# Kernel tuning notes

Measured on AMD Instinct MI355X. Metric: run time of the kernel, lower is better.

Reference implementation:

```python
import jax, jax.numpy as jnp
import numpy as np

N_EMBD = 1024
N_HEAD = 16
D_HEAD = N_EMBD // N_HEAD
B, T = 4, 2048


def _layernorm(x, g, b, eps=1e-5):
    mu = jnp.mean(x, axis=-1, keepdims=True)
    var = jnp.var(x, axis=-1, keepdims=True)
    return (x - mu) * jax.lax.rsqrt(var + eps) * g + b


def setup_inputs() -> dict:
    key = jax.random.key(0)
    ks = jax.random.split(key, 16)
    C = N_EMBD
    s = 0.02
    return {
        "x": jax.random.normal(ks[0], (B, T, C), jnp.float32),
        "ln1_g": jnp.ones((C,), jnp.float32),
        "ln1_b": jnp.zeros((C,), jnp.float32),
        "Wq": jax.random.normal(ks[1], (C, C), jnp.float32) * s,
        "bq": jnp.zeros((C,), jnp.float32),
        "Wk": jax.random.normal(ks[2], (C, C), jnp.float32) * s,
        "bk": jnp.zeros((C,), jnp.float32),
        "Wv": jax.random.normal(ks[3], (C, C), jnp.float32) * s,
        "bv": jnp.zeros((C,), jnp.float32),
        "Wo": jax.random.normal(ks[4], (C, C), jnp.float32) * s,
        "bo": jnp.zeros((C,), jnp.float32),
        "ln2_g": jnp.ones((C,), jnp.float32),
        "ln2_b": jnp.zeros((C,), jnp.float32),
        "W1": jax.random.normal(ks[5], (C, 4 * C), jnp.float32) * s,
        "b1": jnp.zeros((4 * C,), jnp.float32),
        "W2": jax.random.normal(ks[6], (4 * C, C), jnp.float32) * s,
        "b2": jnp.zeros((C,), jnp.float32),
    }


def reference(x, ln1_g, ln1_b, Wq, bq, Wk, bk, Wv, bv, Wo, bo,
              ln2_g, ln2_b, W1, b1, W2, b2):
    Bx, Tx, C = x.shape
    H, D = N_HEAD, D_HEAD

    # --- attention (pre-LN) ---
    h = _layernorm(x, ln1_g, ln1_b)
    q = (h @ Wq + bq).reshape(Bx, Tx, H, D)
    k = (h @ Wk + bk).reshape(Bx, Tx, H, D)
    v = (h @ Wv + bv).reshape(Bx, Tx, H, D)
    att = jnp.einsum("bqhd,bkhd->bhqk", q, k) * (1.0 / jnp.sqrt(jnp.float32(D)))
    causal = jnp.tril(jnp.ones((Tx, Tx), bool))
    att = jnp.where(causal, att, -jnp.inf)
    att = jax.nn.softmax(att, axis=-1)
    y = jnp.einsum("bhqk,bkhd->bqhd", att, v).reshape(Bx, Tx, C)
    x = x + (y @ Wo + bo)

    # --- MLP (pre-LN), exact GELU as in torch F.gelu default ---
    h2 = _layernorm(x, ln2_g, ln2_b)
    m = jax.nn.gelu(h2 @ W1 + b1, approximate=False)
    x = x + (m @ W2 + b2)
    return x
```

## Files before the change

kernel.cpp:

```cpp
#include <hip/hip_runtime.h>
#include <hip/hip_bf16.h>
#include <math.h>

#define C_EMBD 1024
#define T_SEQ  2048
#define BATCH  4
#define NHEAD  16
#define DHEAD  64

typedef __attribute__((ext_vector_type(8))) short bf16x8;
typedef __attribute__((ext_vector_type(4))) float floatx4;

#if __has_builtin(__builtin_amdgcn_exp2f)
#define EXP2F __builtin_amdgcn_exp2f
#else
#define EXP2F exp2f
#endif

static __device__ __forceinline__ floatx4 mfma16(bf16x8 a, bf16x8 b, floatx4 c) {
    return __builtin_amdgcn_mfma_f32_16x16x32_bf16(a, b, c, 0, 0, 0);
}

static __device__ __forceinline__ void gl2lds16(const void* g, void* l) {
    __builtin_amdgcn_global_load_lds(
        (const __attribute__((address_space(1))) void*)g,
        (__attribute__((address_space(3))) void*)l, 16, 0, 0);
}

__global__ __launch_bounds__(256) void transpose_cvt(
        const float* __restrict__ W, __hip_bfloat16* __restrict__ Wt, int K, int N) {
    __shared__ float tile[32][33];
    const int tid = threadIdx.x;
    const int n0 = blockIdx.x * 32, k0 = blockIdx.y * 32;
    const int r = tid >> 3, c4 = (tid & 7) * 4;
    float4 v = *(const float4*)&W[(size_t)(k0 + r) * N + n0 + c4];
    tile[r][c4 + 0] = v.x; tile[r][c4 + 1] = v.y;
    tile[r][c4 + 2] = v.z; tile[r][c4 + 3] = v.w;
    __syncthreads();
    __align__(8) __hip_bfloat16 ob[4];
    ob[0] = __float2bfloat16(tile[c4 + 0][r]);
    ob[1] = __float2bfloat16(tile[c4 + 1][r]);
    ob[2] = __float2bfloat16(tile[c4 + 2][r]);
    ob[3] = __float2bfloat16(tile[c4 + 3][r]);
    *(short4*)&Wt[(size_t)(n0 + r) * K + k0 + c4] = *(short4*)ob;
}

__global__ __launch_bounds__(256) void ln_bf16(
        const float* __restrict__ x, const float* __restrict__ g,
        const float* __restrict__ b, __hip_bfloat16* __restrict__ out) {
    const int row = blockIdx.x, tid = threadIdx.x;
    const float4 v = ((const float4*)(x + (size_t)row * C_EMBD))[tid];
    float s  = v.x + v.y + v.z + v.w;
    float sq = v.x * v.x + v.y * v.y + v.z * v.z + v.w * v.w;
    #pragma unroll
    for (int off = 1; off < 64; off <<= 1) {
        s  += __shfl_xor(s, off);
        sq += __shfl_xor(sq, off);
    }
    __shared__ float ps[4], pq[4];
    if ((tid & 63) == 0) { ps[tid >> 6] = s; pq[tid >> 6] = sq; }
    __syncthreads();
    s  = ps[0] + ps[1] + ps[2] + ps[3];
    sq = pq[0] + pq[1] + pq[2] + pq[3];
    const float mu   = s * (1.0f / C_EMBD);
    const float var  = sq * (1.0f / C_EMBD) - mu * mu;
    const float rstd = rsqrtf(var + 1e-5f);
    const float4 gv = ((const float4*)g)[tid];
    const float4 bv = ((const float4*)b)[tid];
    __align__(8) __hip_bfloat16 ob[4];
    ob[0] = __float2bfloat16((v.x - mu) * rstd * gv.x + bv.x);
    ob[1] = __float2bfloat16((v.y - mu) * rstd * gv.y + bv.y);
    ob[2] = __float2bfloat16((v.z - mu) * rstd * gv.z + bv.z);
    ob[3] = __float2bfloat16((v.w - mu) * rstd * gv.w + bv.w);
    *(short4*)&out[(size_t)row * C_EMBD + tid * 4] = *(short4*)ob;
}

template <int EP>
__global__ __launch_bounds__(256, 2) void gemm_bt(
        const __hip_bfloat16* __restrict__ A, const __hip_bfloat16* __restrict__ Bt,
        int M, int N, int K,
        const float* __restrict__ ba, const float* __restrict__ bb, const float* __restrict__ bc,
        __hip_bfloat16* __restrict__ o0, __hip_bfloat16* __restrict__ o1,
        __hip_bfloat16* __restrict__ o2, float* __restrict__ of,
        const float* __restrict__ resid) {
    __shared__ __align__(16) __hip_bfloat16 As[2][128 * 32];
    __shared__ __align__(16) __hip_bfloat16 Bs[2][128 * 32];
    const int tid  = threadIdx.x;

    const int gx  = gridDim.x;
    const int nwg = gx * gridDim.y;
    const int lin = blockIdx.x + gx * blockIdx.y;
    const int cpx = nwg >> 3;
    const int wg  = (lin & 7) * cpx + (lin >> 3);
    const int by  = (wg & 7) + 8 * (wg / (gx << 3));
    const int bx  = (wg >> 3) % gx;
    const int n0  = bx * 128;
    const int m0  = by * 128;

    const int wave = tid >> 6, lane = tid & 63;
    const int l15  = lane & 15, quad = lane >> 4;
    const int wm   = (wave & 1) * 64, wn = (wave >> 1) * 64;
    const int c0   = wave * 2;
    const int sr   = lane >> 2;
    const int sc   = (lane & 3) * 8;

    const floatx4 z4 = {0.f, 0.f, 0.f, 0.f};
    floatx4 acc[4][4];
    #pragma unroll
    for (int i = 0; i < 4; i++)
        #pragma unroll
        for (int j = 0; j < 4; j++) acc[i][j] = z4;

    auto stage = [&](const int buf, const int k0) {
        gl2lds16(&A [(m0 + c0 * 16 + sr) * K + k0 + sc],       &As[buf][c0 * 512]);
        gl2lds16(&A [(m0 + (c0 + 1) * 16 + sr) * K + k0 + sc], &As[buf][(c0 + 1) * 512]);
        gl2lds16(&Bt[(n0 + c0 * 16 + sr) * K + k0 + sc],       &Bs[buf][c0 * 512]);
        gl2lds16(&Bt[(n0 + (c0 + 1) * 16 + sr) * K + k0 + sc], &Bs[buf][(c0 + 1) * 512]);
    };

    stage(0, 0);
    const int nk = K >> 5;
    for (int t = 0; t < nk; ++t) {
        const int cur = t & 1;
        if (t + 1 < nk) {
            stage(cur ^ 1, (t + 1) * 32);
            asm volatile("s_waitcnt vmcnt(4)" ::: "memory");
        } else {
            asm volatile("s_waitcnt vmcnt(0)" ::: "memory");
        }
        __builtin_amdgcn_s_barrier();
        asm volatile("" ::: "memory");
        bf16x8 af[4], bfr[4];
        #pragma unroll
        for (int i = 0; i < 4; i++)
            af[i] = *(const bf16x8*)&As[cur][(wm + i * 16 + l15) * 32 + quad * 8];
        #pragma unroll
        for (int j = 0; j < 4; j++)
            bfr[j] = *(const bf16x8*)&Bs[cur][(wn + j * 16 + l15) * 32 + quad * 8];
        #pragma unroll
        for (int i = 0; i < 4; i++)
            #pragma unroll
            for (int j = 0; j < 4; j++)
                acc[i][j] = mfma16(af[i], bfr[j], acc[i][j]);
        asm volatile("" ::: "memory");
        __builtin_amdgcn_s_barrier();
    }

    #pragma unroll
    for (int i = 0; i < 4; i++) {
        #pragma unroll
        for (int j = 0; j < 4; j++) {
            const int col = n0 + wn + j * 16 + l15;
            #pragma unroll
            for (int r = 0; r < 4; r++) {
                const int m = m0 + wm + i * 16 + quad * 4 + r;
                float val = acc[i][j][r];
                if (EP == 1) {
                    val += ba[col];
                    of[m * N + col] = resid[m * N + col] + val;
                } else {
                    val += ba[col];
                    of[m * N + col] += val;
                }
            }
        }
    }
}

template <int EP>
__global__ __launch_bounds__(512, 2) void gemm256_8ph(
        const __hip_bfloat16* __restrict__ A, const __hip_bfloat16* __restrict__ Bt,
        int M, int N, int K,
        const float* __restrict__ ba, const float* __restrict__ bb, const float* __restrict__ bc,
        __hip_bfloat16* __restrict__ o0, __hip_bfloat16* __restrict__ o1,
        __hip_bfloat16* __restrict__ o2) {
    __shared__ __align__(16) __hip_bfloat16 As[2][256 * 64];
    __shared__ __align__(16) __hip_bfloat16 Bs[2][256 * 64];
    const int tid = threadIdx.x;

    const int gx  = gridDim.x;
    const int nwg = gx * gridDim.y;
    const int lin = blockIdx.x + gx * blockIdx.y;
    const int cpx = nwg >> 3;
    const int wg  = (lin & 7) * cpx + (lin >> 3);
    const int by  = (wg & 7) + 8 * (wg / (gx << 3));
    const int bx  = (wg >> 3) % gx;
    const int n0  = bx * 256;
    const int m0  = by * 256;

    const int wave = tid >> 6, lane = tid & 63;
    const int l15 = lane & 15, quad = lane >> 4;
    const int wr  = wave >> 2, wc = wave & 3;
    const int swz = l15 & 7;
    const int sr8 = tid >> 3;
    const int sg  = (tid & 7) ^ (sr8 & 7);

    const floatx4 z4 = {0.f, 0.f, 0.f, 0.f};
    floatx4 acc[8][4];
    #pragma unroll
    for (int i = 0; i < 8; i++)
        #pragma unroll
        for (int j = 0; j < 4; j++) acc[i][j] = z4;

    auto stA = [&](const int buf, const int half, const int k0) {
        #pragma unroll
        for (int s = 0; s < 2; s++) {
            const int r0 = half * 128 + s * 64;
            gl2lds16(&A[(size_t)(m0 + r0 + sr8) * K + k0 + sg * 8],
                     &As[buf][r0 * 64 + wave * 512]);
        }
    };
    auto stB = [&](const int buf, const int half, const int k0) {
        #pragma unroll
        for (int s = 0; s < 2; s++) {
            const int r0 = half * 128 + s * 64;
            gl2lds16(&Bt[(size_t)(n0 + r0 + sr8) * K + k0 + sg * 8],
                     &Bs[buf][r0 * 64 + wave * 512]);
        }
    };
    auto ldA = [&](const int buf, const int mi, const int ks) -> bf16x8 {
        return *(const bf16x8*)&As[buf][(mi * 32 + wr * 16 + l15) * 64 +
                                        (((ks * 4 + quad) ^ swz) * 8)];
    };
    auto ldB = [&](const int buf, const int nj, const int ks) -> bf16x8 {
        return *(const bf16x8*)&Bs[buf][(wc * 64 + nj * 16 + l15) * 64 +
                                        (((ks * 4 + quad) ^ swz) * 8)];
    };

    const int NT = K >> 6;
    stA(0, 0, 0); stB(0, 0, 0); stA(0, 1, 0); stB(0, 1, 0);
    stA(1, 0, 64); stB(1, 0, 64);
    asm volatile("s_waitcnt vmcnt(4)" ::: "memory");
    __builtin_amdgcn_s_barrier();
    asm volatile("" ::: "memory");

    for (int t = 0; t < NT; ++t) {
        const int cur = t & 1;
        const int kn1 = (t + 1) * 64, kn2 = (t + 2) * 64;
        const bool s1 = (t + 1 < NT), s2 = (t + 2 < NT);
        bf16x8 bfrag[4][2];
        #pragma unroll
        for (int p = 0; p < 4; ++p) {
            bf16x8 afr[2][2];
            if (p == 0) {
                #pragma unroll
                for (int nj = 0; nj < 4; nj++)
                    #pragma unroll
                    for (int ks = 0; ks < 2; ks++)
                        bfrag[nj][ks] = ldB(cur, nj, ks);
            }
            #pragma unroll
            for (int i = 0; i < 2; i++)
                #pragma unroll
                for (int ks = 0; ks < 2; ks++)
                    afr[i][ks] = ldA(cur, 2 * p + i, ks);
            if (p == 0)      { if (s1) stA(cur ^ 1, 1, kn1); }
            else if (p == 1) { if (s1) stB(cur ^ 1, 1, kn1); }
            else if (p == 2) { if (s2) stA(cur, 0, kn2); }
            else             { if (s2) stB(cur, 0, kn2); }
            asm volatile("" ::: "memory");
            __builtin_amdgcn_s_barrier();
            asm volatile("s_waitcnt lgkmcnt(0)" ::: "memory");
            __builtin_amdgcn_s_setprio(1);
            #pragma unroll
            for (int i = 0; i < 2; i++)
                #pragma unroll
                for (int nj = 0; nj < 4; nj++)
                    #pragma unroll
                    for (int ks = 0; ks < 2; ks++)
                        acc[2 * p + i][nj] = mfma16(afr[i][ks], bfrag[nj][ks], acc[2 * p + i][nj]);
            __builtin_amdgcn_s_setprio(0);
            if (p == 3) {
                if (s2) { asm volatile("s_waitcnt vmcnt(4)" ::: "memory"); }
                else    { asm volatile("s_waitcnt vmcnt(0)" ::: "memory"); }
            }
            asm volatile("" ::: "memory");
            __builtin_amdgcn_s_barrier();
            asm volatile("" ::: "memory");
        }
    }

    #pragma unroll
    for (int mi = 0; mi < 8; mi++) {
        #pragma unroll
        for (int nj = 0; nj < 4; nj++) {
            const int col = n0 + wc * 64 + nj * 16 + l15;
            #pragma unroll
            for (int r = 0; r < 4; r++) {
                const int m = m0 + mi * 32 + wr * 16 + quad * 4 + r;
                float val = acc[mi][nj][r];
                if (EP == 0) {
                    const int which = col >> 10, cn = col & 1023;
                    const float* bp = (which == 0) ? ba : (which == 1) ? bb : bc;
                    val += bp[cn];
                    const int head = cn >> 6, d = cn & 63;
                    const int bidx = m >> 11, tt = m & 2047;
                    if (which == 0) {
                        val *= 0.18033688011112042f;
                        o0[((bidx * NHEAD + head) * T_SEQ + tt) * DHEAD + d] = __float2bfloat16(val);
                    } else if (which == 1) {
                        o1[((bidx * NHEAD + head) * T_SEQ + tt) * DHEAD + d] = __float2bfloat16(val);
                    } else {
                        o2[((bidx * NHEAD + head) * DHEAD + d) * T_SEQ + tt] = __float2bfloat16(val);
                    }
                } else {
                    val += ba[col];
                    const float gl = 0.5f * val * (1.0f + erff(val * 0.70710678118654752f));
                    o0[(size_t)m * N + col] = __float2bfloat16(gl);
                }
            }
        }
    }
}

__global__ __launch_bounds__(256, 2) void attn_fa(
        const __hip_bfloat16* __restrict__ q, const __hip_bfloat16* __restrict__ k,
        const __hip_bfloat16* __restrict__ vt, __hip_bfloat16* __restrict__ y) {
    __shared__ __align__(16) __hip_bfloat16 Ks[2][64 * 64];
    __shared__ __align__(16) __hip_bfloat16 Vs[2][64 * 64];
    __shared__ __align__(16) __hip_bfloat16 pl[4][32 * 72];
    const int tid = threadIdx.x;
    const int wave = tid >> 6, lane = tid & 63;
    const int l15 = lane & 15, quad = lane >> 4;
    const int sw  = l15 & 7;
    const int lr  = lane >> 3;
    const int gsw = (lane & 7) ^ lr;

    const int lin  = blockIdx.x;
    const int xcd  = lin & 7;
    const int slot = lin >> 3;
    const int bh   = xcd * 8 + (slot >> 3);
    const int jA   = slot & 7;

    const __hip_bfloat16* qp = q + (size_t)bh * T_SEQ * DHEAD;
    const __hip_bfloat16* kp = k + (size_t)bh * T_SEQ * DHEAD;
    const __hip_bfloat16* vp = vt + (size_t)bh * DHEAD * T_SEQ;
    __hip_bfloat16* myp = &pl[wave][0];
    const int b = bh >> 4, head = bh & 15;
    const floatx4 z4 = {0.f, 0.f, 0.f, 0.f};

    auto stage = [&](const int buf, const int kb) {
        #pragma unroll
        for (int j = 0; j < 2; j++) {
            const int rb = wave * 16 + j * 8;
            gl2lds16(&kp[(size_t)(kb + rb + lr) * DHEAD + gsw * 8], &Ks[buf][rb * 64]);
            gl2lds16(&vp[(size_t)(rb + lr) * T_SEQ + kb + gsw * 8], &Vs[buf][rb * 64]);
        }
    };

    auto segment = [&](const int tile) {
        const int q0 = tile * 128;
        const int qw = q0 + wave * 32;
        const int cc = tile * 2 + 1;

        bf16x8 bq[2][2];
        #pragma unroll
        for (int qi = 0; qi < 2; qi++)
            #pragma unroll
            for (int h = 0; h < 2; h++)
                bq[qi][h] = *(const bf16x8*)&qp[(qw + qi * 16 + l15) * DHEAD + h * 32 + quad * 8];

        floatx4 oac[2][4];
        #pragma unroll
        for (int qi = 0; qi < 2; qi++)
            #pragma unroll
            for (int nd = 0; nd < 4; nd++) oac[qi][nd] = z4;
        float li[2] = {0.f, 0.f};

        stage(0, 0);

        for (int t = 0; t <= cc; t++) {
            const int cur = t & 1;
            if (t < cc) {
                stage(cur ^ 1, (t + 1) * 64);
                asm volatile("s_waitcnt vmcnt(4)" ::: "memory");
            } else {
                asm volatile("s_waitcnt vmcnt(0)" ::: "memory");
            }
            __builtin_amdgcn_s_barrier();
            asm volatile("" ::: "memory");

            const int kb = t * 64;
            const bool act = (kb <= qw + 31);
            if (act) {
                const bool dg = (kb + 63 > qw);
                bf16x8 kf[4][2];
                #pragma unroll
                for (int nt = 0; nt < 4; nt++)
                    #pragma unroll
                    for (int h = 0; h < 2; h++)
                        kf[nt][h] = *(const bf16x8*)&Ks[cur][(nt * 16 + l15) * 64 + (((h * 4 + quad) ^ sw) * 8)];
                floatx4 sa[2][4];
                #pragma unroll
                for (int qi = 0; qi < 2; qi++)
                    #pragma unroll
                    for (int nt = 0; nt < 4; nt++) sa[qi][nt] = z4;
                #pragma unroll
                for (int nt = 0; nt < 4; nt++)
                    #pragma unroll
                    for (int h = 0; h < 2; h++) {
                        sa[0][nt] = mfma16(kf[nt][h], bq[0][h], sa[0][nt]);
                        sa[1][nt] = mfma16(kf[nt][h], bq[1][h], sa[1][nt]);
                    }
                if (dg) {
                    #pragma unroll
                    for (int qi = 0; qi < 2; qi++)
                        #pragma unroll
                        for (int nt = 0; nt < 4; nt++)
                            #pragma unroll
                            for (int r = 0; r < 4; r++)
                                if (kb + nt * 16 + quad * 4 + r > qw + qi * 16 + l15)
                                    sa[qi][nt][r] = -INFINITY;
                }
                #pragma unroll
                for (int qi = 0; qi < 2; qi++) {
                    float sm = 0.f;
                    #pragma unroll
                    for (int nt = 0; nt < 4; nt++) {
                        __align__(8) __hip_bfloat16 pk[4];
                        #pragma unroll
                        for (int r = 0; r < 4; r++) {
                            const float p = EXP2F(sa[qi][nt][r]);
                            sm += p;
                            pk[r] = __float2bfloat16(p);
                        }
                        *(short4*)&myp[(qi * 16 + l15) * 72 + nt * 16 + quad * 4] = *(short4*)pk;
                    }
                    li[qi] += sm;
                }
                bf16x8 vf[4][2];
                #pragma unroll
                for (int nd = 0; nd < 4; nd++)
                    #pragma unroll
                    for (int kh = 0; kh < 2; kh++)
                        vf[nd][kh] = *(const bf16x8*)&Vs[cur][(nd * 16 + l15) * 64 + (((kh * 4 + quad) ^ sw) * 8)];
                asm volatile("s_waitcnt lgkmcnt(0)" ::: "memory");
                bf16x8 pf[2][2];
                #pragma unroll
                for (int qi = 0; qi < 2; qi++)
                    #pragma unroll
                    for (int kh = 0; kh < 2; kh++)
                        pf[qi][kh] = *(const bf16x8*)&myp[(qi * 16 + l15) * 72 + kh * 32 + quad * 8];
                #pragma unroll
                for (int nd = 0; nd < 4; nd++)
                    #pragma unroll
                    for (int kh = 0; kh < 2; kh++) {
                        oac[0][nd] = mfma16(vf[nd][kh], pf[0][kh], oac[0][nd]);
                        oac[1][nd] = mfma16(vf[nd][kh], pf[1][kh], oac[1][nd]);
                    }
            }
            asm volatile("" ::: "memory");
            __builtin_amdgcn_s_barrier();
        }

        float inv[2];
        #pragma unroll
        for (int qi = 0; qi < 2; qi++) {
            float l = li[qi];
            l += __shfl_xor(l, 16);
            l += __shfl_xor(l, 32);
            inv[qi] = 1.0f / l;
        }
        #pragma unroll
        for (int qi = 0; qi < 2; qi++)
            #pragma unroll
            for (int nd = 0; nd < 4; nd++) {
                __align__(8) __hip_bfloat16 ok[4];
                #pragma unroll
                for (int r = 0; r < 4; r++) ok[r] = __float2bfloat16(oac[qi][nd][r] * inv[qi]);
                *(short4*)&myp[(qi * 16 + l15) * 72 + nd * 16 + quad * 4] = *(short4*)ok;
            }
        asm volatile("s_waitcnt lgkmcnt(0)" ::: "memory");
        #pragma unroll
        for (int half = 0; half < 2; half++) {
            const int row = half * 16 + (lane >> 2);
            const int cb  = (lane & 3) * 16;
            const bf16x8 v0 = *(const bf16x8*)&myp[row * 72 + cb];
            const bf16x8 v1 = *(const bf16x8*)&myp[row * 72 + cb + 8];
            __hip_bfloat16* yr = &y[(size_t)(b * T_SEQ + qw + row) * C_EMBD + head * DHEAD + cb];
            *(bf16x8*)yr       = v0;
            *(bf16x8*)(yr + 8) = v1;
        }
        asm volatile("s_waitcnt vmcnt(0)" ::: "memory");
    };

    segment(jA);
    segment(15 - jA);
}

extern "C" void kernel_launch(void* const* d_in, const int* in_sizes, int n_in,
                              void* d_out, int out_size, void* d_ws, size_t ws_size,
                              hipStream_t stream) {
    const float* x     = (const float*)d_in[0];
    const float* ln1_g = (const float*)d_in[1];
    const float* ln1_b = (const float*)d_in[2];
    const float* Wq    = (const float*)d_in[3];
    const float* bq    = (const float*)d_in[4];
    const float* Wk    = (const float*)d_in[5];
    const float* bk    = (const float*)d_in[6];
    const float* Wv    = (const float*)d_in[7];
    const float* bv    = (const float*)d_in[8];
    const float* Wo    = (const float*)d_in[9];
    const float* bo    = (const float*)d_in[10];
    const float* ln2_g = (const float*)d_in[11];
    const float* ln2_b = (const float*)d_in[12];
    const float* W1    = (const float*)d_in[13];
    const float* b1    = (const float*)d_in[14];
    const float* W2    = (const float*)d_in[15];
    const float* b2    = (const float*)d_in[16];
    float* out = (float*)d_out;

    char* ws = (char*)d_ws;
    __hip_bfloat16* wqkvt = (__hip_bfloat16*)(ws);
    __hip_bfloat16* wot   = (__hip_bfloat16*)(ws + 6291456);
    __hip_bfloat16* w1t   = (__hip_bfloat16*)(ws + 8388608);
    __hip_bfloat16* w2t   = (__hip_bfloat16*)(ws + 16777216);
    __hip_bfloat16* hbuf  = (__hip_bfloat16*)(ws + 25165824);
    __hip_bfloat16* qbuf  = (__hip_bfloat16*)(ws + 41943040);
    __hip_bfloat16* kbuf  = (__hip_bfloat16*)(ws + 58720256);
    __hip_bfloat16* vbuf  = (__hip_bfloat16*)(ws + 75497472);
    __hip_bfloat16* ybuf  = (__hip_bfloat16*)(ws + 92274688);
    __hip_bfloat16* mbuf  = (__hip_bfloat16*)(ws + 41943040);

    transpose_cvt<<<dim3(32, 32), 256, 0, stream>>>(Wq, wqkvt, 1024, 1024);
    transpose_cvt<<<dim3(32, 32), 256, 0, stream>>>(Wk, wqkvt + 1024 * 1024, 1024, 1024);
    transpose_cvt<<<dim3(32, 32), 256, 0, stream>>>(Wv, wqkvt + 2048 * 1024, 1024, 1024);
    transpose_cvt<<<dim3(32, 32), 256, 0, stream>>>(Wo, wot, 1024, 1024);
    transpose_cvt<<<dim3(128, 32), 256, 0, stream>>>(W1, w1t, 1024, 4096);
    transpose_cvt<<<dim3(32, 128), 256, 0, stream>>>(W2, w2t, 4096, 1024);

    ln_bf16<<<8192, 256, 0, stream>>>(x, ln1_g, ln1_b, hbuf);

    gemm256_8ph<0><<<dim3(12, 32), 512, 0, stream>>>(hbuf, wqkvt, 8192, 3072, 1024,
        bq, bk, bv, qbuf, kbuf, vbuf);

    attn_fa<<<dim3(512), 256, 0, stream>>>(qbuf, kbuf, vbuf, ybuf);

    gemm_bt<1><<<dim3(8, 64), 256, 0, stream>>>(ybuf, wot, 8192, 1024, 1024,
        bo, nullptr, nullptr, nullptr, nullptr, nullptr, out, x);

    ln_bf16<<<8192, 256, 0, stream>>>(out, ln2_g, ln2_b, hbuf);

    gemm256_8ph<2><<<dim3(16, 32), 512, 0, stream>>>(hbuf, w1t, 8192, 4096, 1024,
        b1, nullptr, nullptr, mbuf, nullptr, nullptr);

    gemm_bt<3><<<dim3(8, 64), 256, 0, stream>>>(mbuf, w2t, 8192, 1024, 4096,
        b2, nullptr, nullptr, nullptr, nullptr, nullptr, out, nullptr);
}
```

Baseline: 544.7 us.

## Stage GEMM epilogue through LDS for coalesced 16-byte stores; merge transposes

```diff
diff --git a/kernel.cpp b/kernel.cpp
--- a/kernel.cpp
+++ b/kernel.cpp
@@ -43,6 +43,31 @@
     ob[2] = __float2bfloat16(tile[c4 + 2][r]);
     ob[3] = __float2bfloat16(tile[c4 + 3][r]);
     *(short4*)&Wt[(size_t)(n0 + r) * K + k0 + c4] = *(short4*)ob;
+}
+
+__global__ __launch_bounds__(256) void transpose_cvt4(
+        const float* __restrict__ W0, const float* __restrict__ W1_,
+        const float* __restrict__ W2_, const float* __restrict__ W3_,
+        __hip_bfloat16* __restrict__ T0, __hip_bfloat16* __restrict__ T1,
+        __hip_bfloat16* __restrict__ T2, __hip_bfloat16* __restrict__ T3) {
+    __shared__ float tile[32][33];
+    const float* W = (blockIdx.z == 0) ? W0 : (blockIdx.z == 1) ? W1_ :
+                     (blockIdx.z == 2) ? W2_ : W3_;
+    __hip_bfloat16* Wt = (blockIdx.z == 0) ? T0 : (blockIdx.z == 1) ? T1 :
+                         (blockIdx.z == 2) ? T2 : T3;
+    const int tid = threadIdx.x;
+    const int n0 = blockIdx.x * 32, k0 = blockIdx.y * 32;
+    const int r = tid >> 3, c4 = (tid & 7) * 4;
+    float4 v = *(const float4*)&W[(size_t)(k0 + r) * 1024 + n0 + c4];
+    tile[r][c4 + 0] = v.x; tile[r][c4 + 1] = v.y;
+    tile[r][c4 + 2] = v.z; tile[r][c4 + 3] = v.w;
+    __syncthreads();
+    __align__(8) __hip_bfloat16 ob[4];
+    ob[0] = __float2bfloat16(tile[c4 + 0][r]);
+    ob[1] = __float2bfloat16(tile[c4 + 1][r]);
+    ob[2] = __float2bfloat16(tile[c4 + 2][r]);
+    ob[3] = __float2bfloat16(tile[c4 + 3][r]);
+    *(short4*)&Wt[(size_t)(n0 + r) * 1024 + k0 + c4] = *(short4*)ob;
 }
 
 __global__ __launch_bounds__(256) void ln_bf16(
@@ -280,35 +305,84 @@
         }
     }
 
-    #pragma unroll
-    for (int mi = 0; mi < 8; mi++) {
-        #pragma unroll
-        for (int nj = 0; nj < 4; nj++) {
-            const int col = n0 + wc * 64 + nj * 16 + l15;
-            #pragma unroll
-            for (int r = 0; r < 4; r++) {
-                const int m = m0 + mi * 32 + wr * 16 + quad * 4 + r;
-                float val = acc[mi][nj][r];
-                if (EP == 0) {
-                    const int which = col >> 10, cn = col & 1023;
-                    const float* bp = (which == 0) ? ba : (which == 1) ? bb : bc;
-                    val += bp[cn];
-                    const int head = cn >> 6, d = cn & 63;
-                    const int bidx = m >> 11, tt = m & 2047;
-                    if (which == 0) {
-                        val *= 0.18033688011112042f;
-                        o0[((bidx * NHEAD + head) * T_SEQ + tt) * DHEAD + d] = __float2bfloat16(val);
-                    } else if (which == 1) {
-                        o1[((bidx * NHEAD + head) * T_SEQ + tt) * DHEAD + d] = __float2bfloat16(val);
-                    } else {
-                        o2[((bidx * NHEAD + head) * DHEAD + d) * T_SEQ + tt] = __float2bfloat16(val);
+    __hip_bfloat16* slab = (wc < 2) ? (&As[0][0] + wc * 16384)
+                                    : (&Bs[0][0] + (wc - 2) * 16384);
+    const int lid = wr * 64 + lane;
+
+    if (EP == 0) {
+        const int which = n0 >> 10;
+        const int cn0   = (n0 & 1023) + wc * 64;
+        const int head  = cn0 >> 6;
+        const int bidx  = m0 >> 11;
+        const int t0    = m0 & 2047;
+        const float* bp = (which == 0) ? ba : (which == 1) ? bb : bc;
+        float bias[4];
+        #pragma unroll
+        for (int nj = 0; nj < 4; nj++) bias[nj] = bp[cn0 + nj * 16 + l15];
+        if (which < 2) {
+            const float scale = (which == 0) ? 0.18033688011112042f : 1.0f;
+            #pragma unroll
+            for (int mi = 0; mi < 8; mi++)
+                #pragma unroll
+                for (int nj = 0; nj < 4; nj++)
+                    #pragma unroll
+                    for (int r = 0; r < 4; r++) {
+                        const int row = mi * 32 + wr * 16 + quad * 4 + r;
+                        slab[row * 64 + nj * 16 + l15] =
+                            __float2bfloat16((acc[mi][nj][r] + bias[nj]) * scale);
                     }
-                } else {
-                    val += ba[col];
+            __syncthreads();
+            __hip_bfloat16* dst = ((which == 0) ? o0 : o1) +
+                ((size_t)(bidx * NHEAD + head) * T_SEQ + t0) * DHEAD;
+            #pragma unroll
+            for (int s = 0; s < 16; s++)
+                *(bf16x8*)&dst[s * 1024 + lid * 8] = *(const bf16x8*)&slab[s * 1024 + lid * 8];
+        } else {
+            #pragma unroll
+            for (int mi = 0; mi < 8; mi++)
+                #pragma unroll
+                for (int nj = 0; nj < 4; nj++) {
+                    const int d   = nj * 16 + l15;
+                    const int key = (d & 7) << 3;
+                    #pragma unroll
+                    for (int r = 0; r < 4; r++) {
+                        const int row = mi * 32 + wr * 16 + quad * 4 + r;
+                        slab[d * 256 + (row ^ key)] =
+                            __float2bfloat16(acc[mi][nj][r] + bias[nj]);
+                    }
+                }
+            __syncthreads();
+            __hip_bfloat16* dst = o2 + (size_t)(bidx * NHEAD + head) * DHEAD * T_SEQ + t0;
+            const int dly = lid >> 5;
+            const int tly = (lid & 31) * 8;
+            #pragma unroll
+            for (int s = 0; s < 16; s++) {
+                const int d = s * 4 + dly;
+                *(bf16x8*)&dst[(size_t)d * T_SEQ + tly] =
+                    *(const bf16x8*)&slab[d * 256 + (tly ^ ((d & 7) << 3))];
+            }
+        }
+    } else {
+        float bias[4];
+        #pragma unroll
+        for (int nj = 0; nj < 4; nj++) bias[nj] = ba[n0 + wc * 64 + nj * 16 + l15];
+        #pragma unroll
+        for (int mi = 0; mi < 8; mi++)
+            #pragma unroll
+            for (int nj = 0; nj < 4; nj++)
+                #pragma unroll
+                for (int r = 0; r < 4; r++) {
+                    const int row = mi * 32 + wr * 16 + quad * 4 + r;
+                    const float val = acc[mi][nj][r] + bias[nj];
                     const float gl = 0.5f * val * (1.0f + erff(val * 0.70710678118654752f));
-                    o0[(size_t)m * N + col] = __float2bfloat16(gl);
+                    slab[row * 64 + nj * 16 + l15] = __float2bfloat16(gl);
                 }
-            }
+        __syncthreads();
+        #pragma unroll
+        for (int s = 0; s < 16; s++) {
+            const int row = s * 16 + (lid >> 3);
+            *(bf16x8*)&o0[(size_t)(m0 + row) * N + n0 + wc * 64 + (lid & 7) * 8] =
+                *(const bf16x8*)&slab[row * 64 + (lid & 7) * 8];
         }
     }
 }
@@ -522,10 +596,8 @@
     __hip_bfloat16* ybuf  = (__hip_bfloat16*)(ws + 92274688);
     __hip_bfloat16* mbuf  = (__hip_bfloat16*)(ws + 41943040);
 
-    transpose_cvt<<<dim3(32, 32), 256, 0, stream>>>(Wq, wqkvt, 1024, 1024);
-    transpose_cvt<<<dim3(32, 32), 256, 0, stream>>>(Wk, wqkvt + 1024 * 1024, 1024, 1024);
-    transpose_cvt<<<dim3(32, 32), 256, 0, stream>>>(Wv, wqkvt + 2048 * 1024, 1024, 1024);
-    transpose_cvt<<<dim3(32, 32), 256, 0, stream>>>(Wo, wot, 1024, 1024);
+    transpose_cvt4<<<dim3(32, 32, 4), 256, 0, stream>>>(
+        Wq, Wk, Wv, Wo, wqkvt, wqkvt + 1024 * 1024, wqkvt + 2048 * 1024, wot);
     transpose_cvt<<<dim3(128, 32), 256, 0, stream>>>(W1, w1t, 1024, 4096);
     transpose_cvt<<<dim3(32, 128), 256, 0, stream>>>(W2, w2t, 4096, 1024);
 
```

Result: faster. 513.9 us (-5.7%).
